# Kernel optimization log

Hardware: AMD Instinct MI355X
Metric: run time of the kernel (lower is better)

The kernel has to match this reference:

```python
import jax, jax.numpy as jnp
import numpy as np

N_NODES = 100000
N_EDGES = 1600000
HID = 256
HEADS = 4
HEAD_DIM = HID // HEADS
EPS = 1e-5


def _layernorm(x, g, b):
    mu = jnp.mean(x, axis=-1, keepdims=True)
    var = jnp.mean(jnp.square(x - mu), axis=-1, keepdims=True)
    return (x - mu) * jax.lax.rsqrt(var + EPS) * g + b


def setup_inputs() -> dict:
    key = jax.random.key(0)
    ks = jax.random.split(key, 16)
    s = 0.05  # small init, mimics xavier gain=0.1
    inp = {
        'h': jax.random.normal(ks[0], (N_NODES, HID), jnp.float32),
        'src': jax.random.randint(ks[1], (N_EDGES,), 0, N_NODES, jnp.int32),
        'dst': jax.random.randint(ks[2], (N_EDGES,), 0, N_NODES, jnp.int32),
        'Wq': jax.random.normal(ks[3], (HID, HID), jnp.float32) * s,
        'bq': jnp.zeros((HID,), jnp.float32),
        'Wk': jax.random.normal(ks[4], (HID, HID), jnp.float32) * s,
        'bk': jnp.zeros((HID,), jnp.float32),
        'Wv': jax.random.normal(ks[5], (HID, HID), jnp.float32) * s,
        'bv': jnp.zeros((HID,), jnp.float32),
        'Wo': jax.random.normal(ks[6], (HID, HID), jnp.float32) * s,
        'bo': jnp.zeros((HID,), jnp.float32),
        'W1': jax.random.normal(ks[7], (HID, 2 * HID), jnp.float32) * s,
        'b1': jnp.zeros((2 * HID,), jnp.float32),
        'W2': jax.random.normal(ks[8], (2 * HID, HID), jnp.float32) * s,
        'b2': jnp.zeros((HID,), jnp.float32),
        'g1': jnp.ones((HID,), jnp.float32),
        'be1': jnp.zeros((HID,), jnp.float32),
        'g2': jnp.ones((HID,), jnp.float32),
        'be2': jnp.zeros((HID,), jnp.float32),
    }
    return inp


def reference(h, src, dst, Wq, bq, Wk, bk, Wv, bv, Wo, bo, W1, b1, W2, b2, g1, be1, g2, be2):
    N = h.shape[0]
    scale = HEAD_DIM ** -0.5
    h_norm = _layernorm(h, g1, be1)
    Q = (h_norm @ Wq + bq).reshape(N, HEADS, HEAD_DIM)
    K = (h_norm @ Wk + bk).reshape(N, HEADS, HEAD_DIM)
    V = (h_norm @ Wv + bv).reshape(N, HEADS, HEAD_DIM)

    # per-edge attention logits: q from dst, k from src  -> [E, heads]
    logits = jnp.einsum('ehd,ehd->eh', Q[dst], K[src]) * scale

    # edge softmax grouped by destination node (dgl.ops.edge_softmax)
    seg_max = jax.ops.segment_max(logits, dst, num_segments=N)  # [N, heads]
    e = jnp.exp(logits - seg_max[dst])
    seg_sum = jax.ops.segment_sum(e, dst, num_segments=N)
    w = e / seg_sum[dst]  # [E, heads]

    # message = V[src] * attn ; aggregate by sum over incoming edges
    msg = V[src] * w[:, :, None]  # [E, heads, head_dim]
    h_new = jax.ops.segment_sum(msg, dst, num_segments=N).reshape(N, HID)

    h_attn = h_new @ Wo + bo
    h = h + h_attn  # dropout is identity in eval
    h2 = _layernorm(h, g2, be2)
    ffn = jax.nn.relu(h2 @ W1 + b1) @ W2 + b2
    return h + ffn
```

## Files before the change

kernel.cpp:

```cpp
#include <hip/hip_runtime.h>
#include <hip/hip_bf16.h>

#define NN 100000
#define NE 1600000

typedef __attribute__((ext_vector_type(8))) short bf16x8;
typedef __attribute__((ext_vector_type(4))) float f32x4;
typedef __attribute__((ext_vector_type(2))) float f32x2;
typedef __attribute__((ext_vector_type(2))) unsigned int u32x2;
typedef __attribute__((ext_vector_type(4))) unsigned int u32x4;

__device__ __forceinline__ float bf2f(unsigned short u) {
    union { unsigned int i; float f; } c; c.i = ((unsigned int)u) << 16; return c.f;
}
__device__ __forceinline__ unsigned short f2bf(float f) {
    union { float f; unsigned int i; } c; c.f = f;
    unsigned int lsb = (c.i >> 16) & 1u;
    c.i += 0x7FFFu + lsb;
    return (unsigned short)(c.i >> 16);
}
__device__ __forceinline__ u32x4 pack8bf(f32x4 a, f32x4 b) {
    u32x4 p;
    p.x = f2bf(a[0]) | ((unsigned int)f2bf(a[1]) << 16);
    p.y = f2bf(a[2]) | ((unsigned int)f2bf(a[3]) << 16);
    p.z = f2bf(b[0]) | ((unsigned int)f2bf(b[1]) << 16);
    p.w = f2bf(b[2]) | ((unsigned int)f2bf(b[3]) << 16);
    return p;
}
__device__ __forceinline__ unsigned int pack4fp8(f32x4 v) {
    unsigned int w = __builtin_amdgcn_cvt_pk_fp8_f32(v[0], v[1], 0, false);
    return __builtin_amdgcn_cvt_pk_fp8_f32(v[2], v[3], w, true);
}
__device__ __forceinline__ void gload_lds16(const void* g, void* l) {
    __builtin_amdgcn_global_load_lds(
        (const __attribute__((address_space(1))) void*)g,
        (__attribute__((address_space(3))) void*)l, 16, 0, 0);
}

__global__ __launch_bounds__(256) void ln_k(
    const float* __restrict__ x, const float* __restrict__ g,
    const float* __restrict__ b, unsigned short* __restrict__ y, int nrows)
{
    int w = threadIdx.x >> 6, lane = threadIdx.x & 63;
    int row = blockIdx.x * 4 + w;
    if (row >= nrows) return;
    const float4 xv = *(const float4*)(x + (size_t)row * 256 + lane * 4);
    float s  = xv.x + xv.y + xv.z + xv.w;
    float sq = xv.x*xv.x + xv.y*xv.y + xv.z*xv.z + xv.w*xv.w;
    #pragma unroll
    for (int m = 1; m < 64; m <<= 1) {
        s  += __shfl_xor(s,  m);
        sq += __shfl_xor(sq, m);
    }
    float mu  = s * (1.0f / 256.0f);
    float var = sq * (1.0f / 256.0f) - mu * mu;
    float r = rsqrtf(var + 1e-5f);
    float4 gv = *(const float4*)(g + lane * 4);
    float4 bv = *(const float4*)(b + lane * 4);
    ushort4 o;
    o.x = f2bf((xv.x - mu) * r * gv.x + bv.x);
    o.y = f2bf((xv.y - mu) * r * gv.y + bv.y);
    o.z = f2bf((xv.z - mu) * r * gv.z + bv.z);
    o.w = f2bf((xv.w - mu) * r * gv.w + bv.w);
    *(ushort4*)(y + (size_t)row * 256 + lane * 4) = o;
}

__global__ __launch_bounds__(256) void wcv_all_k(
    const float* __restrict__ Wq, const float* __restrict__ Wk, const float* __restrict__ Wv,
    const float* __restrict__ Wo, const float* __restrict__ W1, const float* __restrict__ W2,
    unsigned short* __restrict__ Wqkvt, unsigned short* __restrict__ Wot,
    unsigned short* __restrict__ W1t, unsigned short* __restrict__ W2t,
    const float* __restrict__ bq, const float* __restrict__ bk, const float* __restrict__ bv,
    float* __restrict__ bqkv)
{
    int id = blockIdx.x;
    int t = threadIdx.x;
    if (id == 512) {
        bqkv[t] = bq[t]; bqkv[256 + t] = bk[t]; bqkv[512 + t] = bv[t];
        return;
    }
    const float* W; unsigned short* Wt; int K, N, kx, ny;
    if (id < 192) {
        int grp = id >> 6, l = id & 63;
        W = (grp == 0) ? Wq : ((grp == 1) ? Wk : Wv);
        Wt = Wqkvt + grp * 256 * 256;
        K = 256; N = 256; kx = l & 7; ny = l >> 3;
    } else if (id < 256) {
        int l = id - 192; W = Wo; Wt = Wot; K = 256; N = 256; kx = l & 7; ny = l >> 3;
    } else if (id < 384) {
        int l = id - 256; W = W1; Wt = W1t; K = 256; N = 512; kx = l & 7; ny = l >> 3;
    } else {
        int l = id - 384; W = W2; Wt = W2t; K = 512; N = 256; kx = l & 15; ny = l >> 4;
    }
    __shared__ unsigned short tl[32][33];
    int bk2 = kx * 32, bn = ny * 32;
    int lx = t & 31, ly = t >> 5;
    #pragma unroll
    for (int r = 0; r < 32; r += 8)
        tl[ly + r][lx] = f2bf(W[(size_t)(bk2 + ly + r) * N + bn + lx]);
    __syncthreads();
    #pragma unroll
    for (int r = 0; r < 32; r += 8)
        Wt[(size_t)(bn + ly + r) * K + bk2 + lx] = tl[lx][ly + r];
}

template<int NBX, int OMODE, bool RELU, bool RES>
__global__ __launch_bounds__(512) void mgemm_k(
    const unsigned short* __restrict__ A, const unsigned short* __restrict__ Wt,
    const float* __restrict__ bias, void* __restrict__ outv, void* __restrict__ out2,
    const void* __restrict__ res, const float* __restrict__ g, const float* __restrict__ be,
    int M, int N, int K)
{
    __shared__ __align__(16) char lds[73728];
    const int t = threadIdx.x;
    const int lane = t & 63;
    const int wid = t >> 6;
    const int wm = wid >> 2, wn = wid & 3;

    int bmi, bni;
    if (NBX > 0) {
        const int nwg = gridDim.x;
        const int q = nwg >> 3, r = nwg & 7;
        const int xcd = blockIdx.x & 7, idx = blockIdx.x >> 3;
        const int wgid = (xcd < r) ? (xcd * (q + 1) + idx)
                                   : (r * (q + 1) + (xcd - r) * q + idx);
        bmi = wgid / NBX; bni = wgid - bmi * NBX;
    } else {
        bmi = blockIdx.y; bni = blockIdx.x;
    }
    const int bm = bmi * 128, bn = bni * 256;

    f32x4 acc[4][4] = {};

    const int ra_s = t >> 2;
    const int sa_s = (t & 3) ^ (ra_s & 3);
    const size_t arow = (size_t)min(bm + ra_s, M - 1) * K + sa_s * 8;
    const int rb0 = t >> 2;
    const int sb0 = (t & 3) ^ (rb0 & 3);
    const int rb1 = (512 + t) >> 2;
    const int sb1 = (t & 3) ^ (rb1 & 3);
    const size_t brow0 = (size_t)(bn + rb0) * K + sb0 * 8;
    const size_t brow1 = (size_t)(bn + rb1) * K + sb1 * 8;

    const int fr = lane & 15, fs = lane >> 4;
    const int rslot = fs ^ (fr & 3);

    const int KS = K >> 5;

#define STAGE(b, k0) { \
        unsigned short* Ab = (unsigned short*)(lds + (b) * 8192); \
        unsigned short* Bb = (unsigned short*)(lds + 24576 + (b) * 16384); \
        const int kk_ = (k0) << 5; \
        gload_lds16(A + arow + kk_, Ab + t * 8); \
        gload_lds16(Wt + brow0 + kk_, Bb + t * 8); \
        gload_lds16(Wt + brow1 + kk_, Bb + (512 + t) * 8); }

    STAGE(0, 0)
    STAGE(1, 1)
    int cur = 0;
    for (int ks = 0; ks < KS; ++ks) {
        if (ks + 1 < KS) asm volatile("s_waitcnt vmcnt(3)" ::: "memory");
        else             asm volatile("s_waitcnt vmcnt(0)" ::: "memory");
        __builtin_amdgcn_s_barrier();
        if (ks + 2 < KS) {
            int nb = cur + 2; if (nb >= 3) nb -= 3;
            STAGE(nb, ks + 2)
        }
        const unsigned short* As = (const unsigned short*)(lds + cur * 8192);
        const unsigned short* Bs = (const unsigned short*)(lds + 24576 + cur * 16384);
        bf16x8 af[4], bf[4];
        #pragma unroll
        for (int fm = 0; fm < 4; ++fm)
            af[fm] = *(const bf16x8*)&As[(wm * 64 + fm * 16 + fr) * 32 + rslot * 8];
        #pragma unroll
        for (int fn = 0; fn < 4; ++fn)
            bf[fn] = *(const bf16x8*)&Bs[(wn * 64 + fn * 16 + fr) * 32 + rslot * 8];
        #pragma unroll
        for (int fm = 0; fm < 4; ++fm)
            #pragma unroll
            for (int fn = 0; fn < 4; ++fn)
                acc[fm][fn] = __builtin_amdgcn_mfma_f32_16x16x32_bf16(
                    af[fm], bf[fn], acc[fm][fn], 0, 0, 0);
        if (++cur == 3) cur = 0;
    }
#undef STAGE
    __syncthreads();

    float* wl = (float*)(lds + wid * 4352);
    float* stats = (float*)(lds + 34816);
    const int rr = lane >> 2;
    const int c4 = (lane & 3) * 16;
    const int qg = lane >> 4;

    #pragma unroll
    for (int fm = 0; fm < 4; ++fm) {
        #pragma unroll
        for (int fn = 0; fn < 4; ++fn)
            #pragma unroll
            for (int i = 0; i < 4; ++i)
                wl[(qg * 4 + i) * 68 + fn * 16 + fr] = acc[fm][fn][i];
        f32x4 v0 = *(const f32x4*)&wl[rr * 68 + c4 + 0];
        f32x4 v1 = *(const f32x4*)&wl[rr * 68 + c4 + 4];
        f32x4 v2 = *(const f32x4*)&wl[rr * 68 + c4 + 8];
        f32x4 v3 = *(const f32x4*)&wl[rr * 68 + c4 + 12];
        const int rowg = bm + wm * 64 + fm * 16 + rr;
        const int colg = bn + wn * 64 + c4;
        if (rowg < M) {
            v0 += *(const f32x4*)&bias[colg + 0];
            v1 += *(const f32x4*)&bias[colg + 4];
            v2 += *(const f32x4*)&bias[colg + 8];
            v3 += *(const f32x4*)&bias[colg + 12];
            if (RES) {
                if (OMODE == 4) {
                    const unsigned short* rp = (const unsigned short*)res + (size_t)rowg * N + colg;
                    u32x4 ra = *(const u32x4*)rp;
                    u32x4 rb = *(const u32x4*)(rp + 8);
                    v0[0] += bf2f(ra.x & 0xffff); v0[1] += bf2f(ra.x >> 16);
                    v0[2] += bf2f(ra.y & 0xffff); v0[3] += bf2f(ra.y >> 16);
                    v1[0] += bf2f(ra.z & 0xffff); v1[1] += bf2f(ra.z >> 16);
                    v1[2] += bf2f(ra.w & 0xffff); v1[3] += bf2f(ra.w >> 16);
                    v2[0] += bf2f(rb.x & 0xffff); v2[1] += bf2f(rb.x >> 16);
                    v2[2] += bf2f(rb.y & 0xffff); v2[3] += bf2f(rb.y >> 16);
                    v3[0] += bf2f(rb.z & 0xffff); v3[1] += bf2f(rb.z >> 16);
                    v3[2] += bf2f(rb.w & 0xffff); v3[3] += bf2f(rb.w >> 16);
                } else {
                    const float* rp = (const float*)res + (size_t)rowg * N + colg;
                    v0 += *(const f32x4*)(rp + 0);
                    v1 += *(const f32x4*)(rp + 4);
                    v2 += *(const f32x4*)(rp + 8);
                    v3 += *(const f32x4*)(rp + 12);
                }
            }
            if (RELU) {
                #pragma unroll
                for (int j = 0; j < 4; ++j) {
                    v0[j] = fmaxf(v0[j], 0.f); v1[j] = fmaxf(v1[j], 0.f);
                    v2[j] = fmaxf(v2[j], 0.f); v3[j] = fmaxf(v3[j], 0.f);
                }
            }
        } else {
            v0 = 0.f; v1 = 0.f; v2 = 0.f; v3 = 0.f;
        }

        if (OMODE == 3) {
            acc[fm][0] = v0; acc[fm][1] = v1; acc[fm][2] = v2; acc[fm][3] = v3;
        } else if (rowg < M) {
            if (OMODE == 0 || OMODE == 4) {
                float* op = (float*)outv + (size_t)rowg * N + colg;
                *(f32x4*)(op + 0) = v0; *(f32x4*)(op + 4) = v1;
                *(f32x4*)(op + 8) = v2; *(f32x4*)(op + 12) = v3;
            } else if (OMODE == 1) {
                unsigned short* op = (unsigned short*)outv + (size_t)rowg * N + colg;
                *(u32x4*)(op + 0) = pack8bf(v0, v1);
                *(u32x4*)(op + 8) = pack8bf(v2, v3);
            } else {
                if (colg < 256) {
                    unsigned short* op = (unsigned short*)outv + (size_t)rowg * 256 + colg;
                    *(u32x4*)(op + 0) = pack8bf(v0, v1);
                    *(u32x4*)(op + 8) = pack8bf(v2, v3);
                } else {
                    u32x4 p8;
                    p8.x = pack4fp8(v0); p8.y = pack4fp8(v1);
                    p8.z = pack4fp8(v2); p8.w = pack4fp8(v3);
                    *(u32x4*)((unsigned char*)out2 + (size_t)rowg * 512 + (colg - 256)) = p8;
                }
            }
        }
    }

    if (OMODE == 3) {
        #pragma unroll
        for (int fm = 0; fm < 4; ++fm) {
            float s = 0.f, q = 0.f;
            #pragma unroll
            for (int j = 0; j < 4; ++j)
                #pragma unroll
                for (int c = 0; c < 4; ++c) {
                    float x = acc[fm][j][c];
                    s += x; q += x * x;
                }
            s += __shfl_xor(s, 1); q += __shfl_xor(q, 1);
            s += __shfl_xor(s, 2); q += __shfl_xor(q, 2);
            if ((lane & 3) == 0) {
                int rowl = wm * 64 + fm * 16 + rr;
                stats[rowl * 8 + wn * 2 + 0] = s;
                stats[rowl * 8 + wn * 2 + 1] = q;
            }
        }
        __syncthreads();
        #pragma unroll
        for (int fm = 0; fm < 4; ++fm) {
            const int rowl = wm * 64 + fm * 16 + rr;
            const int rowg = bm + rowl;
            float s = stats[rowl * 8 + 0] + stats[rowl * 8 + 2] + stats[rowl * 8 + 4] + stats[rowl * 8 + 6];
            float q = stats[rowl * 8 + 1] + stats[rowl * 8 + 3] + stats[rowl * 8 + 5] + stats[rowl * 8 + 7];
            float mu = s * (1.0f / 256.0f);
            float var = q * (1.0f / 256.0f) - mu * mu;
            float rstd = rsqrtf(var + 1e-5f);
            const int colg = bn + wn * 64 + c4;
            if (rowg < M) {
                unsigned short* mp = (unsigned short*)out2 + (size_t)rowg * 256 + colg;
                *(u32x4*)(mp + 0) = pack8bf(acc[fm][0], acc[fm][1]);
                *(u32x4*)(mp + 8) = pack8bf(acc[fm][2], acc[fm][3]);
                f32x4 nv[4];
                #pragma unroll
                for (int j = 0; j < 4; ++j) {
                    f32x4 gv = *(const f32x4*)&g[colg + j * 4];
                    f32x4 bv = *(const f32x4*)&be[colg + j * 4];
                    #pragma unroll
                    for (int c = 0; c < 4; ++c)
                        nv[j][c] = (acc[fm][j][c] - mu) * rstd * gv[c] + bv[c];
                }
                unsigned short* op = (unsigned short*)outv + (size_t)rowg * 256 + colg;
                *(u32x4*)(op + 0) = pack8bf(nv[0], nv[1]);
                *(u32x4*)(op + 8) = pack8bf(nv[2], nv[3]);
            }
        }
    }
}

__global__ void degcnt_k(const int* __restrict__ dst, int* __restrict__ deg, int E)
{
    int e = blockIdx.x * blockDim.x + threadIdx.x;
    if (e < E) atomicAdd(deg + dst[e], 1);
}

__global__ __launch_bounds__(1024) void scanA_k(int* __restrict__ a, int* __restrict__ aux, int n)
{
    __shared__ int wsum[16];
    __shared__ int wpre[16];
    int t = threadIdx.x, lane = t & 63, w = t >> 6;
    int i = blockIdx.x * 1024 + t;
    int v = (i < n) ? a[i] : 0;
    int s = v;
    #pragma unroll
    for (int d = 1; d < 64; d <<= 1) {
        int u = __shfl_up(s, d);
        if (lane >= d) s += u;
    }
    if (lane == 63) wsum[w] = s;
    __syncthreads();
    if (t == 0) {
        int run = 0;
        #pragma unroll
        for (int j = 0; j < 16; ++j) { wpre[j] = run; run += wsum[j]; }
        aux[blockIdx.x] = run;
    }
    __syncthreads();
    if (i < n) a[i] = wpre[w] + s - v;
}

__global__ __launch_bounds__(128) void scanB_k(int* __restrict__ aux, int* __restrict__ tot, int nb)
{
    __shared__ int ws[2];
    int t = threadIdx.x, lane = t & 63, w = t >> 6;
    int v = (t < nb) ? aux[t] : 0;
    int s = v;
    #pragma unroll
    for (int d = 1; d < 64; d <<= 1) {
        int u = __shfl_up(s, d);
        if (lane >= d) s += u;
    }
    if (lane == 63) ws[w] = s;
    __syncthreads();
    int add = (w == 1) ? ws[0] : 0;
    if (t < nb) aux[t] = add + s - v;
    if (t == nb - 1) tot[0] = add + s;
}

__global__ __launch_bounds__(1024) void scanC_k(int* __restrict__ a, const int* __restrict__ aux, int n)
{
    int i = blockIdx.x * 1024 + threadIdx.x;
    if (i < n) a[i] += aux[blockIdx.x];
}

__global__ void scatter_k(
    const int* __restrict__ dst, const int* __restrict__ srcarr,
    const int* __restrict__ off, int* __restrict__ cursor,
    int* __restrict__ csr, int E)
{
    int e = blockIdx.x * blockDim.x + threadIdx.x;
    if (e >= E) return;
    int d = dst[e];
    int pos = off[d] + atomicAdd(cursor + d, 1);
    csr[pos] = srcarr[e];
}

__global__ __launch_bounds__(256) void attn_k(
    const int* __restrict__ csr, const int* __restrict__ off,
    const unsigned short* __restrict__ Q, const unsigned char* __restrict__ KV8,
    unsigned short* __restrict__ hnew)
{
    int w = threadIdx.x >> 6, lane = threadIdx.x & 63;
    int n = blockIdx.x * 4 + w;
    if (n >= NN) return;
    int e0 = off[n], e1 = off[n + 1];
    int hl = lane & 31, par = lane >> 5;

    const float qs = 0.125f * 1.4426950408889634f;
    f32x2 q01, q23, q45, q67;
    {
        u32x4 qa = __builtin_nontemporal_load((const u32x4*)(Q + (size_t)n * 256 + hl * 8));
        q01[0] = bf2f((unsigned short)(qa.x & 0xffff)) * qs;
        q01[1] = bf2f((unsigned short)(qa.x >> 16)) * qs;
        q23[0] = bf2f((unsigned short)(qa.y & 0xffff)) * qs;
        q23[1] = bf2f((unsigned short)(qa.y >> 16)) * qs;
        q45[0] = bf2f((unsigned short)(qa.z & 0xffff)) * qs;
        q45[1] = bf2f((unsigned short)(qa.z >> 16)) * qs;
        q67[0] = bf2f((unsigned short)(qa.w & 0xffff)) * qs;
        q67[1] = bf2f((unsigned short)(qa.w >> 16)) * qs;
    }
    f32x2 a01 = {0.f, 0.f}, a23 = {0.f, 0.f}, a45 = {0.f, 0.f}, a67 = {0.f, 0.f};
    float s = 0.f;
    const unsigned char* KVl = KV8 + hl * 8;

    int i = e0;
    for (; i + 7 < e1; i += 8) {
        int b[4];
        #pragma unroll
        for (int t2 = 0; t2 < 4; ++t2) b[t2] = csr[i + 2 * t2 + par] << 9;
        u32x2 kd[4], vd[4];
        #pragma unroll
        for (int t2 = 0; t2 < 4; ++t2) {
            kd[t2] = *(const u32x2*)(KVl + (unsigned)b[t2]);
            vd[t2] = *(const u32x2*)(KVl + (unsigned)b[t2] + 256);
        }
        #pragma unroll
        for (int t2 = 0; t2 < 4; ++t2) {
            f32x2 lv = q01 * __builtin_amdgcn_cvt_pk_f32_fp8(kd[t2].x, false);
            lv += q23 * __builtin_amdgcn_cvt_pk_f32_fp8(kd[t2].x, true);
            lv += q45 * __builtin_amdgcn_cvt_pk_f32_fp8(kd[t2].y, false);
            lv += q67 * __builtin_amdgcn_cvt_pk_f32_fp8(kd[t2].y, true);
            float l = lv[0] + lv[1];
            l += __shfl_xor(l, 1);
            l += __shfl_xor(l, 2);
            l += __shfl_xor(l, 4);
            float p = exp2f(l);
            s += p;
            f32x2 pp = {p, p};
            a01 += pp * __builtin_amdgcn_cvt_pk_f32_fp8(vd[t2].x, false);
            a23 += pp * __builtin_amdgcn_cvt_pk_f32_fp8(vd[t2].x, true);
            a45 += pp * __builtin_amdgcn_cvt_pk_f32_fp8(vd[t2].y, false);
            a67 += pp * __builtin_amdgcn_cvt_pk_f32_fp8(vd[t2].y, true);
        }
    }
    for (; i < e1; i += 2) {
        int eidx = i + par;
        int idx = (eidx < e1) ? eidx : (e1 - 1);
        int b = csr[idx] << 9;
        u32x2 kd = *(const u32x2*)(KVl + (unsigned)b);
        u32x2 vd = *(const u32x2*)(KVl + (unsigned)b + 256);
        f32x2 lv = q01 * __builtin_amdgcn_cvt_pk_f32_fp8(kd.x, false);
        lv += q23 * __builtin_amdgcn_cvt_pk_f32_fp8(kd.x, true);
        lv += q45 * __builtin_amdgcn_cvt_pk_f32_fp8(kd.y, false);
        lv += q67 * __builtin_amdgcn_cvt_pk_f32_fp8(kd.y, true);
        float l = lv[0] + lv[1];
        l += __shfl_xor(l, 1);
        l += __shfl_xor(l, 2);
        l += __shfl_xor(l, 4);
        float p = (eidx < e1) ? exp2f(l) : 0.f;
        s += p;
        f32x2 pp = {p, p};
        a01 += pp * __builtin_amdgcn_cvt_pk_f32_fp8(vd.x, false);
        a23 += pp * __builtin_amdgcn_cvt_pk_f32_fp8(vd.x, true);
        a45 += pp * __builtin_amdgcn_cvt_pk_f32_fp8(vd.y, false);
        a67 += pp * __builtin_amdgcn_cvt_pk_f32_fp8(vd.y, true);
    }

    a01[0] += __shfl_xor(a01[0], 32); a01[1] += __shfl_xor(a01[1], 32);
    a23[0] += __shfl_xor(a23[0], 32); a23[1] += __shfl_xor(a23[1], 32);
    a45[0] += __shfl_xor(a45[0], 32); a45[1] += __shfl_xor(a45[1], 32);
    a67[0] += __shfl_xor(a67[0], 32); a67[1] += __shfl_xor(a67[1], 32);
    s += __shfl_xor(s, 32);

    float inv = (e1 > e0) ? 1.0f / s : 0.f;
    if (par == 0) {
        u32x4 ov;
        ov.x = f2bf(a01[0] * inv) | ((unsigned int)f2bf(a01[1] * inv) << 16);
        ov.y = f2bf(a23[0] * inv) | ((unsigned int)f2bf(a23[1] * inv) << 16);
        ov.z = f2bf(a45[0] * inv) | ((unsigned int)f2bf(a45[1] * inv) << 16);
        ov.w = f2bf(a67[0] * inv) | ((unsigned int)f2bf(a67[1] * inv) << 16);
        __builtin_nontemporal_store(ov, (u32x4*)(hnew + (size_t)n * 256 + hl * 8));
    }
}

extern "C" void kernel_launch(void* const* d_in, const int* in_sizes, int n_in,
                              void* d_out, int out_size, void* d_ws, size_t ws_size,
                              hipStream_t stream)
{
    if (n_in < 19) return;
    const float* h   = (const float*)d_in[0];
    const int*   src = (const int*)d_in[1];
    const int*   dst = (const int*)d_in[2];
    const float* Wq  = (const float*)d_in[3];
    const float* bq  = (const float*)d_in[4];
    const float* Wk  = (const float*)d_in[5];
    const float* bk  = (const float*)d_in[6];
    const float* Wv  = (const float*)d_in[7];
    const float* bv  = (const float*)d_in[8];
    const float* Wo  = (const float*)d_in[9];
    const float* bo  = (const float*)d_in[10];
    const float* W1  = (const float*)d_in[11];
    const float* b1  = (const float*)d_in[12];
    const float* W2  = (const float*)d_in[13];
    const float* b2  = (const float*)d_in[14];
    const float* g1  = (const float*)d_in[15];
    const float* be1 = (const float*)d_in[16];
    const float* g2  = (const float*)d_in[17];
    const float* be2 = (const float*)d_in[18];
    float* out = (float*)d_out;

    char* w = (char*)d_ws;
    unsigned short* hnormb = (unsigned short*)(w + 0);
    unsigned short* Qb     = (unsigned short*)(w + 51200000);
    unsigned char*  KV8    = (unsigned char*)(w + 102400000);
    int*            degoff = (int*)(w + 153600000);
    int*            cursor = (int*)(w + 154000384);
    int*            csr    = (int*)(w + 154400768);
    unsigned short* Wqkvt  = (unsigned short*)(w + 204800000);
    unsigned short* Wot    = (unsigned short*)(w + 205193216);
    unsigned short* W1t    = (unsigned short*)(w + 205324288);
    unsigned short* W2t    = (unsigned short*)(w + 205586432);
    float*          bqkv   = (float*)(w + 205848576);
    int*            scanaux= (int*)(w + 205851648);
    unsigned short* hnewb  = hnormb;
    unsigned short* h2nb   = hnormb;
    unsigned short* hmidb  = Qb;
    unsigned short* ffnmid = (unsigned short*)(w + 102400000);

    hipMemsetAsync(degoff, 0, 400384, stream);
    hipMemsetAsync(cursor, 0, 400384, stream);

    const int M = NN;
    dim3 blk(256);
    dim3 blk512(512);
    const int MB = (M + 127) / 128;
    const int SCAN_BLKS = (NN + 1023) / 1024;

    wcv_all_k<<<dim3(513), blk, 0, stream>>>(Wq, Wk, Wv, Wo, W1, W2,
                                             Wqkvt, Wot, W1t, W2t, bq, bk, bv, bqkv);

    degcnt_k<<<dim3((NE + 255) / 256), blk, 0, stream>>>(dst, degoff, NE);
    scanA_k<<<dim3(SCAN_BLKS), dim3(1024), 0, stream>>>(degoff, scanaux, NN);
    scanB_k<<<dim3(1), dim3(128), 0, stream>>>(scanaux, degoff + NN, SCAN_BLKS);
    scanC_k<<<dim3(SCAN_BLKS), dim3(1024), 0, stream>>>(degoff, scanaux, NN);
    scatter_k<<<dim3((NE + 255) / 256), blk, 0, stream>>>(dst, src, degoff, cursor, csr, NE);

    ln_k<<<dim3((NN + 3) / 4), blk, 0, stream>>>(h, g1, be1, hnormb, NN);

    mgemm_k<3, 2, false, false><<<dim3(3 * MB), blk512, 0, stream>>>(
        hnormb, Wqkvt, bqkv, Qb, KV8, nullptr, nullptr, nullptr, M, 768, 256);

    attn_k<<<dim3((NN + 3) / 4), blk, 0, stream>>>(csr, degoff, Qb, KV8, hnewb);

    dim3 go(1, MB);
    mgemm_k<0, 3, false, true><<<go, blk512, 0, stream>>>(
        hnewb, Wot, bo, h2nb, hmidb, h, g2, be2, M, 256, 256);

    mgemm_k<2, 1, true, false><<<dim3(2 * MB), blk512, 0, stream>>>(
        h2nb, W1t, b1, ffnmid, nullptr, nullptr, nullptr, nullptr, M, 512, 256);
    mgemm_k<0, 4, false, true><<<go, blk512, 0, stream>>>(
        ffnmid, W2t, b2, out, nullptr, hmidb, nullptr, nullptr, M, 256, 512);
}
```

Measured before the change: 580.9 us.

## Fuse FFN up and down projections into one kernel keeping intermediate in LDS

Replaces the two FFN GEMM launches (W1 with ReLU writing a bf16 intermediate to global memory, then W2 with residual) with a single kernel. Each 128-row block computes the 512-wide hidden activation in two 256-column halves, stores each half in LDS, and accumulates the W2 product in registers before adding the bias and bf16 residual and writing fp32 output. This removes the global round trip of the 100000x512 intermediate and one launch. In exchange it needs about 160KB of LDS per block, which limits occupancy, and it drops the no-longer-used output modes from the generic GEMM.

Measured after the change: 571.6 us (median of 2 runs). Within noise of the previous version (-1.6%).

```diff
diff --git a/kernel.cpp b/kernel.cpp
--- a/kernel.cpp
+++ b/kernel.cpp
@@ -211,25 +211,11 @@
             v2 += *(const f32x4*)&bias[colg + 8];
             v3 += *(const f32x4*)&bias[colg + 12];
             if (RES) {
-                if (OMODE == 4) {
-                    const unsigned short* rp = (const unsigned short*)res + (size_t)rowg * N + colg;
-                    u32x4 ra = *(const u32x4*)rp;
-                    u32x4 rb = *(const u32x4*)(rp + 8);
-                    v0[0] += bf2f(ra.x & 0xffff); v0[1] += bf2f(ra.x >> 16);
-                    v0[2] += bf2f(ra.y & 0xffff); v0[3] += bf2f(ra.y >> 16);
-                    v1[0] += bf2f(ra.z & 0xffff); v1[1] += bf2f(ra.z >> 16);
-                    v1[2] += bf2f(ra.w & 0xffff); v1[3] += bf2f(ra.w >> 16);
-                    v2[0] += bf2f(rb.x & 0xffff); v2[1] += bf2f(rb.x >> 16);
-                    v2[2] += bf2f(rb.y & 0xffff); v2[3] += bf2f(rb.y >> 16);
-                    v3[0] += bf2f(rb.z & 0xffff); v3[1] += bf2f(rb.z >> 16);
-                    v3[2] += bf2f(rb.w & 0xffff); v3[3] += bf2f(rb.w >> 16);
-                } else {
-                    const float* rp = (const float*)res + (size_t)rowg * N + colg;
-                    v0 += *(const f32x4*)(rp + 0);
-                    v1 += *(const f32x4*)(rp + 4);
-                    v2 += *(const f32x4*)(rp + 8);
-                    v3 += *(const f32x4*)(rp + 12);
-                }
+                const float* rp = (const float*)res + (size_t)rowg * N + colg;
+                v0 += *(const f32x4*)(rp + 0);
+                v1 += *(const f32x4*)(rp + 4);
+                v2 += *(const f32x4*)(rp + 8);
+                v3 += *(const f32x4*)(rp + 12);
             }
             if (RELU) {
                 #pragma unroll
@@ -245,25 +231,15 @@
         if (OMODE == 3) {
             acc[fm][0] = v0; acc[fm][1] = v1; acc[fm][2] = v2; acc[fm][3] = v3;
         } else if (rowg < M) {
-            if (OMODE == 0 || OMODE == 4) {
-                float* op = (float*)outv + (size_t)rowg * N + colg;
-                *(f32x4*)(op + 0) = v0; *(f32x4*)(op + 4) = v1;
-                *(f32x4*)(op + 8) = v2; *(f32x4*)(op + 12) = v3;
-            } else if (OMODE == 1) {
-                unsigned short* op = (unsigned short*)outv + (size_t)rowg * N + colg;
+            if (colg < 256) {
+                unsigned short* op = (unsigned short*)outv + (size_t)rowg * 256 + colg;
                 *(u32x4*)(op + 0) = pack8bf(v0, v1);
                 *(u32x4*)(op + 8) = pack8bf(v2, v3);
             } else {
-                if (colg < 256) {
-                    unsigned short* op = (unsigned short*)outv + (size_t)rowg * 256 + colg;
-                    *(u32x4*)(op + 0) = pack8bf(v0, v1);
-                    *(u32x4*)(op + 8) = pack8bf(v2, v3);
-                } else {
-                    u32x4 p8;
-                    p8.x = pack4fp8(v0); p8.y = pack4fp8(v1);
-                    p8.z = pack4fp8(v2); p8.w = pack4fp8(v3);
-                    *(u32x4*)((unsigned char*)out2 + (size_t)rowg * 512 + (colg - 256)) = p8;
-                }
+                u32x4 p8;
+                p8.x = pack4fp8(v0); p8.y = pack4fp8(v1);
+                p8.z = pack4fp8(v2); p8.w = pack4fp8(v3);
+                *(u32x4*)((unsigned char*)out2 + (size_t)rowg * 512 + (colg - 256)) = p8;
             }
         }
     }
@@ -315,6 +291,171 @@
                 *(u32x4*)(op + 0) = pack8bf(nv[0], nv[1]);
                 *(u32x4*)(op + 8) = pack8bf(nv[2], nv[3]);
             }
+        }
+    }
+}
+
+__global__ __launch_bounds__(512, 2) void mffn_k(
+    const unsigned short* __restrict__ A,
+    const unsigned short* __restrict__ W1t,
+    const unsigned short* __restrict__ W2t,
+    const float* __restrict__ b1, const float* __restrict__ b2,
+    const unsigned short* __restrict__ hmid,
+    float* __restrict__ out, int M)
+{
+    __shared__ __align__(16) char lds[163840];
+    char* Alds = lds;
+    char* Blds = lds + 65536;
+    char* Flds = lds + 98304;
+
+    const int t = threadIdx.x;
+    const int lane = t & 63;
+    const int wid = t >> 6;
+    const int wm = wid >> 2, wn = wid & 3;
+    const int bm = blockIdx.y * 128;
+    const int fr = lane & 15, fs = lane >> 4;
+    const int rslot = fs ^ (fr & 3);
+
+    const int ra = t >> 2;
+    const int sa = (t & 3) ^ (ra & 3);
+    const size_t abase = (size_t)min(bm + ra, M - 1) * 256 + sa * 8;
+    #pragma unroll
+    for (int kc = 0; kc < 8; ++kc)
+        gload_lds16(A + abase + kc * 32, Alds + kc * 8192 + t * 16);
+
+    const int rb0 = t >> 2;
+    const int sb0 = (t & 3) ^ (rb0 & 3);
+    const int rb1 = (512 + t) >> 2;
+    const int sb1 = (t & 3) ^ (rb1 & 3);
+
+    f32x4 acc2[4][4] = {};
+
+    const int rr = lane >> 2;
+    const int qg = lane >> 4;
+
+    for (int nh = 0; nh < 2; ++nh) {
+        f32x4 acc1[4][4] = {};
+        {
+            const unsigned short* B1 = W1t + (size_t)(nh * 256) * 256;
+            gload_lds16(B1 + (size_t)rb0 * 256 + sb0 * 8, Blds + t * 16);
+            gload_lds16(B1 + (size_t)rb1 * 256 + sb1 * 8, Blds + 8192 + t * 16);
+            int cur = 0;
+            for (int ks = 0; ks < 8; ++ks) {
+                __syncthreads();
+                if (ks < 7) {
+                    char* bb = Blds + (cur ^ 1) * 16384;
+                    gload_lds16(B1 + (size_t)rb0 * 256 + sb0 * 8 + (ks + 1) * 32, bb + t * 16);
+                    gload_lds16(B1 + (size_t)rb1 * 256 + sb1 * 8 + (ks + 1) * 32, bb + 8192 + t * 16);
+                }
+                const unsigned short* As = (const unsigned short*)(Alds + ks * 8192);
+                const unsigned short* Bs = (const unsigned short*)(Blds + cur * 16384);
+                bf16x8 af[4], bf[4];
+                #pragma unroll
+                for (int fm = 0; fm < 4; ++fm)
+                    af[fm] = *(const bf16x8*)&As[(wm * 64 + fm * 16 + fr) * 32 + rslot * 8];
+                #pragma unroll
+                for (int fn = 0; fn < 4; ++fn)
+                    bf[fn] = *(const bf16x8*)&Bs[(wn * 64 + fn * 16 + fr) * 32 + rslot * 8];
+                #pragma unroll
+                for (int fm = 0; fm < 4; ++fm)
+                    #pragma unroll
+                    for (int fn = 0; fn < 4; ++fn)
+                        acc1[fm][fn] = __builtin_amdgcn_mfma_f32_16x16x32_bf16(
+                            af[fm], bf[fn], acc1[fm][fn], 0, 0, 0);
+                cur ^= 1;
+            }
+        }
+        __syncthreads();
+
+        {
+            float b1v[4];
+            #pragma unroll
+            for (int fn = 0; fn < 4; ++fn)
+                b1v[fn] = b1[nh * 256 + wn * 64 + fn * 16 + fr];
+            #pragma unroll
+            for (int fm = 0; fm < 4; ++fm)
+                #pragma unroll
+                for (int fn = 0; fn < 4; ++fn)
+                    #pragma unroll
+                    for (int i = 0; i < 4; ++i) {
+                        int row = wm * 64 + fm * 16 + qg * 4 + i;
+                        int col = wn * 64 + fn * 16 + fr;
+                        float v = fmaxf(acc1[fm][fn][i] + b1v[fn], 0.f);
+                        int kc = col >> 5;
+                        int grp = (col >> 3) & 3;
+                        int addr = kc * 8192 + row * 64 + ((grp ^ (row & 3)) * 8 + (col & 7)) * 2;
+                        *(unsigned short*)(Flds + addr) = f2bf(v);
+                    }
+        }
+        __syncthreads();
+
+        {
+            const unsigned short* B2 = W2t + nh * 256;
+            gload_lds16(B2 + (size_t)rb0 * 512 + sb0 * 8, Blds + t * 16);
+            gload_lds16(B2 + (size_t)rb1 * 512 + sb1 * 8, Blds + 8192 + t * 16);
+            int cur = 0;
+            for (int ks = 0; ks < 8; ++ks) {
+                __syncthreads();
+                if (ks < 7) {
+                    char* bb = Blds + (cur ^ 1) * 16384;
+                    gload_lds16(B2 + (size_t)rb0 * 512 + sb0 * 8 + (ks + 1) * 32, bb + t * 16);
+                    gload_lds16(B2 + (size_t)rb1 * 512 + sb1 * 8 + (ks + 1) * 32, bb + 8192 + t * 16);
+                }
+                const unsigned short* Fs = (const unsigned short*)(Flds + ks * 8192);
+                const unsigned short* Bs = (const unsigned short*)(Blds + cur * 16384);
+                bf16x8 af[4], bf[4];
+                #pragma unroll
+                for (int fm = 0; fm < 4; ++fm)
+                    af[fm] = *(const bf16x8*)&Fs[(wm * 64 + fm * 16 + fr) * 32 + rslot * 8];
+                #pragma unroll
+                for (int fn = 0; fn < 4; ++fn)
+                    bf[fn] = *(const bf16x8*)&Bs[(wn * 64 + fn * 16 + fr) * 32 + rslot * 8];
+                #pragma unroll
+                for (int fm = 0; fm < 4; ++fm)
+                    #pragma unroll
+                    for (int fn = 0; fn < 4; ++fn)
+                        acc2[fm][fn] = __builtin_amdgcn_mfma_f32_16x16x32_bf16(
+                            af[fm], bf[fn], acc2[fm][fn], 0, 0, 0);
+                cur ^= 1;
+            }
+        }
+        __syncthreads();
+    }
+
+    float* wl = (float*)(Alds + wid * 4352);
+    const int c4 = (lane & 3) * 16;
+    #pragma unroll
+    for (int fm = 0; fm < 4; ++fm) {
+        #pragma unroll
+        for (int fn = 0; fn < 4; ++fn)
+            #pragma unroll
+            for (int i = 0; i < 4; ++i)
+                wl[(qg * 4 + i) * 68 + fn * 16 + fr] = acc2[fm][fn][i];
+        f32x4 v0 = *(const f32x4*)&wl[rr * 68 + c4 + 0];
+        f32x4 v1 = *(const f32x4*)&wl[rr * 68 + c4 + 4];
+        f32x4 v2 = *(const f32x4*)&wl[rr * 68 + c4 + 8];
+        f32x4 v3 = *(const f32x4*)&wl[rr * 68 + c4 + 12];
+        const int rowg = bm + wm * 64 + fm * 16 + rr;
+        const int colg = wn * 64 + c4;
+        if (rowg < M) {
+            v0 += *(const f32x4*)&b2[colg + 0];
+            v1 += *(const f32x4*)&b2[colg + 4];
+            v2 += *(const f32x4*)&b2[colg + 8];
+            v3 += *(const f32x4*)&b2[colg + 12];
+            const unsigned short* rp = hmid + (size_t)rowg * 256 + colg;
+            u32x4 ra4 = *(const u32x4*)rp;
+            u32x4 rb4 = *(const u32x4*)(rp + 8);
+            v0[0] += bf2f(ra4.x & 0xffff); v0[1] += bf2f(ra4.x >> 16);
+            v0[2] += bf2f(ra4.y & 0xffff); v0[3] += bf2f(ra4.y >> 16);
+            v1[0] += bf2f(ra4.z & 0xffff); v1[1] += bf2f(ra4.z >> 16);
+            v1[2] += bf2f(ra4.w & 0xffff); v1[3] += bf2f(ra4.w >> 16);
+            v2[0] += bf2f(rb4.x & 0xffff); v2[1] += bf2f(rb4.x >> 16);
+            v2[2] += bf2f(rb4.y & 0xffff); v2[3] += bf2f(rb4.y >> 16);
+            v3[0] += bf2f(rb4.z & 0xffff); v3[1] += bf2f(rb4.z >> 16);
+            v3[2] += bf2f(rb4.w & 0xffff); v3[3] += bf2f(rb4.w >> 16);
+            float* op = out + (size_t)rowg * 256 + colg;
+            *(f32x4*)(op + 0) = v0; *(f32x4*)(op + 4) = v1;
+            *(f32x4*)(op + 8) = v2; *(f32x4*)(op + 12) = v3;
         }
     }
 }
@@ -526,7 +667,6 @@
     unsigned short* hnewb  = hnormb;
     unsigned short* h2nb   = hnormb;
     unsigned short* hmidb  = Qb;
-    unsigned short* ffnmid = (unsigned short*)(w + 102400000);
 
     hipMemsetAsync(degoff, 0, 400384, stream);
     hipMemsetAsync(cursor, 0, 400384, stream);
@@ -557,8 +697,5 @@
     mgemm_k<0, 3, false, true><<<go, blk512, 0, stream>>>(
         hnewb, Wot, bo, h2nb, hmidb, h, g2, be2, M, 256, 256);
 
-    mgemm_k<2, 1, true, false><<<dim3(2 * MB), blk512, 0, stream>>>(
-        h2nb, W1t, b1, ffnmid, nullptr, nullptr, nullptr, nullptr, M, 512, 256);
-    mgemm_k<0, 4, false, true><<<go, blk512, 0, stream>>>(
-        ffnmid, W2t, b2, out, nullptr, hmidb, nullptr, nullptr, M, 256, 512);
-}
+    mffn_k<<<go, blk512, 0, stream>>>(h2nb, W1t, W2t, b1, b2, hmidb, out, M);
+}
```
